# Optimization experiments

Measured on AMD Instinct MI355X. Metric: run time of the kernel, lower is better.

The kernel has to match this reference:

```python
import jax, jax.numpy as jnp
import numpy as np

Nc, Nt, B, L = 24, 1024, 32, 24
D = Nt // 4          # 256 encoder_output_dim
C16 = 16 * Nc        # 384 per-channel linears
H8 = 8 * Nc          # 192 LSTM hidden
WS = 0.02            # weight scale for numerical stability


def setup_inputs() -> dict:
    key = jax.random.key(0)
    ctr = [0]
    def nk():
        ctr[0] += 1
        return jax.random.fold_in(key, ctr[0])
    def rn(shape, s=WS):
        return jax.random.normal(nk(), shape, dtype=jnp.float32) * s
    def ru(shape):
        return jax.random.uniform(nk(), shape, dtype=jnp.float32)
    inp = {}
    inp["x"] = rn((B, 1, Nc, Nt), 1.0)
    inp["eps"] = rn((B, C16, L), 1.0)
    inp["sconv_w"] = rn((2 * Nc, 1, Nc, 1)); inp["sconv_b"] = rn((2 * Nc,))
    inp["tconv1_w"] = rn((4 * Nc, 2 * Nc, 1, 16)); inp["tconv1_b"] = rn((4 * Nc,))
    inp["tconv2_w"] = rn((8 * Nc, 4 * Nc, 1, 16)); inp["tconv2_b"] = rn((8 * Nc,))
    for i, c in ((1, 2 * Nc), (2, 4 * Nc), (3, 8 * Nc), (4, 4 * Nc), (5, 2 * Nc), (6, 2 * Nc)):
        inp[f"bn{i}_g"] = ru((c,)); inp[f"bn{i}_b"] = rn((c,))
        inp[f"bn{i}_m"] = jnp.zeros((c,), jnp.float32); inp[f"bn{i}_v"] = jnp.ones((c,), jnp.float32)
        inp[f"a{i}"] = ru((1,))
    for d in ("f", "b"):
        inp[f"w_ih_{d}"] = rn((4 * H8, H8)); inp[f"w_hh_{d}"] = rn((4 * H8, H8))
        inp[f"b_ih_{d}"] = rn((4 * H8,)); inp[f"b_hh_{d}"] = rn((4 * H8,))
    inp["mu_w"] = rn((C16, L, D)); inp["mu_b"] = rn((C16, L))
    inp["lv_w"] = rn((C16, L, D)); inp["lv_b"] = rn((C16, L))
    inp["dec_w"] = rn((C16, D, L)); inp["dec_b"] = rn((C16, D))
    inp["dconv1_w"] = rn((16 * Nc, 4 * Nc, 1, 16)); inp["dconv1_b"] = rn((4 * Nc,))
    inp["dconv2_w"] = rn((8 * Nc, 2 * Nc, 1, 16)); inp["dconv2_b"] = rn((2 * Nc,))
    inp["sdconv_w"] = rn((4 * Nc, 2 * Nc, Nc, 1)); inp["sdconv_b"] = rn((2 * Nc,))
    inp["fconv_w"] = rn((1, 2 * Nc, 1, 1)); inp["fconv_b"] = rn((1,))
    return inp


def _bn(x, g, b, m, v):
    scale = (g * jax.lax.rsqrt(v + 1e-5))[None, :, None, None]
    return (x - m[None, :, None, None]) * scale + b[None, :, None, None]


def _prelu(x, a):
    return jnp.where(x >= 0, x, a * x)


def _conv(x, w, b, stride, pad):
    y = jax.lax.conv_general_dilated(x, w, stride, pad,
                                     dimension_numbers=("NCHW", "OIHW", "NCHW"))
    return y + b[None, :, None, None]


def _convT(x, w, b, stride, pad, opad):
    # w in PyTorch ConvTranspose2d layout (Cin, Cout, kH, kW)
    w2 = jnp.flip(jnp.transpose(w, (1, 0, 2, 3)), (2, 3))
    kH, kW = w.shape[2], w.shape[3]
    padding = ((kH - 1 - pad[0], kH - 1 - pad[0] + opad[0]),
               (kW - 1 - pad[1], kW - 1 - pad[1] + opad[1]))
    y = jax.lax.conv_general_dilated(x, w2, (1, 1), padding, lhs_dilation=stride,
                                     dimension_numbers=("NCHW", "OIHW", "NCHW"))
    return y + b[None, :, None, None]


def _lstm_dir(xs, w_ih, w_hh, b_ih, b_hh, reverse):
    # xs: (T, B, In); PyTorch gate order i, f, g, o
    gx = jnp.einsum("tbi,gi->tbg", xs, w_ih) + (b_ih + b_hh)
    Bb, Hh = xs.shape[1], w_hh.shape[1]
    def step(carry, gt):
        h, c = carry
        gates = gt + h @ w_hh.T
        i, f, g, o = jnp.split(gates, 4, axis=-1)
        c = jax.nn.sigmoid(f) * c + jax.nn.sigmoid(i) * jnp.tanh(g)
        h = jax.nn.sigmoid(o) * jnp.tanh(c)
        return (h, c), h
    init = (jnp.zeros((Bb, Hh), xs.dtype), jnp.zeros((Bb, Hh), xs.dtype))
    _, hs = jax.lax.scan(step, init, gx, reverse=reverse)
    return hs  # (T, B, H), aligned with input time order


def _forward(p):
    # Encoder (dropout = identity, BN in eval mode)
    x1 = _prelu(_bn(_conv(p["x"], p["sconv_w"], p["sconv_b"], (Nc, 1), ((0, 0), (0, 0))),
                    p["bn1_g"], p["bn1_b"], p["bn1_m"], p["bn1_v"]), p["a1"])   # (B,2Nc,1,Nt)
    x2 = _prelu(_bn(_conv(x1, p["tconv1_w"], p["tconv1_b"], (1, 2), ((0, 0), (7, 7))),
                    p["bn2_g"], p["bn2_b"], p["bn2_m"], p["bn2_v"]), p["a2"])   # (B,4Nc,1,Nt/2)
    x3 = _prelu(_bn(_conv(x2, p["tconv2_w"], p["tconv2_b"], (1, 2), ((0, 0), (7, 7))),
                    p["bn3_g"], p["bn3_b"], p["bn3_m"], p["bn3_v"]), p["a3"])   # (B,8Nc,1,Nt/4)
    x3s = jnp.transpose(x3[:, :, 0, :], (2, 0, 1))                              # (T,B,8Nc)
    hf = _lstm_dir(x3s, p["w_ih_f"], p["w_hh_f"], p["b_ih_f"], p["b_hh_f"], False)
    hb = _lstm_dir(x3s, p["w_ih_b"], p["w_hh_b"], p["b_ih_b"], p["b_hh_b"], True)
    h = jnp.concatenate([hf, hb], axis=-1)                                      # (T,B,16Nc)
    h = h.reshape(D, x3.shape[0], H8, 2).mean(-1)                               # AvgPool1d(k=2) over feature dim
    tr = jnp.transpose(h, (1, 2, 0))                                            # (B,8Nc,T)
    e0 = jnp.concatenate([tr, x3[:, :, 0, :]], axis=1)                          # (B,16Nc,T=D)
    # 16*Nc per-channel Linears fused as batched GEMMs
    mu = jnp.einsum("bcd,cld->bcl", e0, p["mu_w"]) + p["mu_b"]                  # (B,384,L)
    logvar = jnp.einsum("bcd,cld->bcl", e0, p["lv_w"]) + p["lv_b"]
    z = mu + p["eps"] * jnp.exp(0.5 * logvar)
    x4 = (jnp.einsum("bcl,cdl->bcd", z, p["dec_w"]) + p["dec_b"])[:, :, None, :]  # (B,384,1,D)
    # Decoder (Nt%4==0 and Nt%2==0 -> output_padding 0)
    u1 = _prelu(_bn(_convT(x4, p["dconv1_w"], p["dconv1_b"], (1, 2), (0, 7), (0, 0)),
                    p["bn4_g"], p["bn4_b"], p["bn4_m"], p["bn4_v"]), p["a4"])   # (B,4Nc,1,Nt/2)
    e1 = jnp.concatenate([u1, x2], axis=1)                                      # (B,8Nc,1,Nt/2)
    u2 = _prelu(_bn(_convT(e1, p["dconv2_w"], p["dconv2_b"], (1, 2), (0, 7), (0, 0)),
                    p["bn5_g"], p["bn5_b"], p["bn5_m"], p["bn5_v"]), p["a5"])   # (B,2Nc,1,Nt)
    e2 = jnp.concatenate([u2, x1], axis=1)                                      # (B,4Nc,1,Nt)
    u3 = _prelu(_bn(_convT(e2, p["sdconv_w"], p["sdconv_b"], (Nc, 1), (0, 0), (0, 0)),
                    p["bn6_g"], p["bn6_b"], p["bn6_m"], p["bn6_v"]), p["a6"])   # (B,2Nc,Nc,Nt)
    out = _conv(u3, p["fconv_w"], p["fconv_b"], (1, 1), ((0, 0), (0, 0)))       # (B,1,Nc,Nt)
    return out, mu, logvar


def reference(x, eps, sconv_w, sconv_b, tconv1_w, tconv1_b, tconv2_w, tconv2_b,
              bn1_g, bn1_b, bn1_m, bn1_v, a1, bn2_g, bn2_b, bn2_m, bn2_v, a2,
              bn3_g, bn3_b, bn3_m, bn3_v, a3, bn4_g, bn4_b, bn4_m, bn4_v, a4,
              bn5_g, bn5_b, bn5_m, bn5_v, a5, bn6_g, bn6_b, bn6_m, bn6_v, a6,
              w_ih_f, w_hh_f, b_ih_f, b_hh_f, w_ih_b, w_hh_b, b_ih_b, b_hh_b,
              mu_w, mu_b, lv_w, lv_b, dec_w, dec_b,
              dconv1_w, dconv1_b, dconv2_w, dconv2_b, sdconv_w, sdconv_b,
              fconv_w, fconv_b):
    p = dict(locals())
    return _forward(p)
```

## Files before the change

### kernel.cpp

```cpp
#include <hip/hip_runtime.h>
#include <cstdint>

#define DI __device__ __forceinline__

typedef __attribute__((ext_vector_type(8))) short s8v;
typedef __attribute__((ext_vector_type(4))) float f4v;
typedef __attribute__((ext_vector_type(4))) uint32_t u4v;

DI float sigmoidf_(float x) {
    return __builtin_amdgcn_rcpf(1.f + __expf(-x));
}
DI float tanhf_(float x) {
    return fmaf(-2.f, __builtin_amdgcn_rcpf(1.f + __expf(2.f * x)), 1.f);
}
DI uint32_t f2bf(float f) {
    uint32_t u = __float_as_uint(f);
    return (u + 0x7fffu + ((u >> 16) & 1u)) >> 16;
}
DI float bflo(uint32_t u) { return __uint_as_float(u << 16); }
DI float bfhi(uint32_t u) { return __uint_as_float(u & 0xffff0000u); }

__global__ __launch_bounds__(256) void k_prep(
    const float* wihf, const float* wihb, const float* whhf, const float* whhb,
    const float* bihf, const float* bhhf, const float* bihb, const float* bhhb,
    const float* sdw,
    float* wihT, uint32_t* wfrag, float* bsum, float* wsdT)
{
    int i = blockIdx.x * 256 + threadIdx.x;
    if (i < 294912) {
        int d = i / 147456, r = i % 147456;
        int ii = r / 768, g = r % 768;
        const float* w = d ? wihb : wihf;
        wihT[i] = w[g * 192 + ii];
        return;
    }
    int j = i - 294912;
    if (j < 147456) {
        int d = j / 73728, r = j % 73728;
        int w = r / 6144, r2 = r % 6144;
        int tau = r2 / 1536, r3 = r2 % 1536;
        int kt = r3 / 256, r4 = r3 % 256;
        int lane = r4 / 4, jp = r4 % 4;
        int n = 16 * (w + 12 * tau) + (lane & 15);
        int k0 = kt * 32 + (lane >> 4) * 8 + jp * 2;
        const float* whh = d ? whhb : whhf;
        uint32_t lo = f2bf(whh[n * 192 + k0]);
        uint32_t hi = f2bf(whh[n * 192 + k0 + 1]);
        wfrag[j] = lo | (hi << 16);
        return;
    }
    int k = j - 147456;
    if (k < 1536) {
        int d = k / 768, g = k % 768;
        bsum[k] = d ? (bihb[g] + bhhb[g]) : (bihf[g] + bhhf[g]);
        return;
    }
    int l = k - 1536;
    if (l < 110592) {
        int h = l / 4608, rem = l % 4608;
        int co = rem / 96, ci = rem % 96;
        wsdT[l] = sdw[(ci * 48 + co) * 24 + h];
    }
}

__global__ __launch_bounds__(256) void k_sconv(
    const float* __restrict__ x, const float* __restrict__ w, const float* __restrict__ bias,
    const float* g, const float* bb, const float* m, const float* v, const float* a,
    float* __restrict__ x1)
{
    int t = blockIdx.x * 256 + threadIdx.x;
    int co = blockIdx.y;
    int b = blockIdx.z;
    const float* xb = x + (size_t)b * 24 * 1024 + t;
    float acc = bias[co];
#pragma unroll
    for (int h = 0; h < 24; ++h) acc = fmaf(xb[h * 1024], w[co * 24 + h], acc);
    float sc = g[co] * rsqrtf(v[co] + 1e-5f);
    float y = (acc - m[co]) * sc + bb[co];
    float al = a[0];
    y = y >= 0.f ? y : al * y;
    x1[((size_t)b * 48 + co) * 1024 + t] = y;
}

template<int CI, int CO, int WOUT, int BSTR>
__global__ __launch_bounds__(256) void k_tconv(
    const float* __restrict__ xin, const float* __restrict__ w, const float* __restrict__ bias,
    const float* g, const float* bb, const float* m, const float* v, const float* a,
    float* __restrict__ out)
{
    const int WIN = WOUT * 2;
    __shared__ float XL[CI][144];
    int tid = threadIdx.x;
    int w0 = blockIdx.x * 64;
    int b = blockIdx.z;
    for (int idx = tid; idx < CI * 144; idx += 256) {
        int ci = idx / 144, p = idx % 144;
        int gp = 2 * w0 - 7 + p;
        XL[ci][p] = (gp >= 0 && gp < WIN) ? xin[((size_t)b * CI + ci) * WIN + gp] : 0.f;
    }
    __syncthreads();
    int tw = tid & 63, cg = tid >> 6;
    int co0 = blockIdx.y * 16 + cg * 4;
    co0 = __builtin_amdgcn_readfirstlane(co0);
    const float* wb = w + (size_t)co0 * CI * 16;
    float acc[4] = {bias[co0], bias[co0 + 1], bias[co0 + 2], bias[co0 + 3]};
    for (int ci = 0; ci < CI; ++ci) {
#pragma unroll
        for (int k = 0; k < 16; ++k) {
            float xv = XL[ci][2 * tw + k];
            acc[0] = fmaf(xv, wb[(0 * CI + ci) * 16 + k], acc[0]);
            acc[1] = fmaf(xv, wb[(1 * CI + ci) * 16 + k], acc[1]);
            acc[2] = fmaf(xv, wb[(2 * CI + ci) * 16 + k], acc[2]);
            acc[3] = fmaf(xv, wb[(3 * CI + ci) * 16 + k], acc[3]);
        }
    }
    float al = a[0];
#pragma unroll
    for (int r = 0; r < 4; ++r) {
        int co = co0 + r;
        float sc = g[co] * rsqrtf(v[co] + 1e-5f);
        float y = (acc[r] - m[co]) * sc + bb[co];
        y = y >= 0.f ? y : al * y;
        out[((size_t)b * BSTR + co) * WOUT + w0 + tw] = y;
    }
}

__global__ __launch_bounds__(256) void k_x3s(const float* __restrict__ e0, float* __restrict__ x3s)
{
    __shared__ float tl[64 * 193];
    int t0 = blockIdx.x * 64, b = blockIdx.y;
    int tid = threadIdx.x;
    for (int idx = tid; idx < 192 * 64; idx += 256) {
        int i = idx >> 6, tt = idx & 63;
        tl[tt * 193 + i] = e0[((size_t)b * 384 + 192 + i) * 256 + t0 + tt];
    }
    __syncthreads();
    for (int idx = tid; idx < 64 * 192; idx += 256) {
        int tt = idx / 192, ii = idx % 192;
        x3s[((size_t)(t0 + tt) * 32 + b) * 192 + ii] = tl[tt * 193 + ii];
    }
}

__global__ __launch_bounds__(256) void k_gemm(
    const float* __restrict__ A, const float* __restrict__ Bm,
    const float* __restrict__ bias, float* __restrict__ C)
{
    __shared__ float AL[64 * 17];
    __shared__ float BL[16 * 68];
    int tid = threadIdx.x;
    int n0 = blockIdx.x * 64, m0 = blockIdx.y * 64;
    int tx = tid & 15, ty = tid >> 4;
    float4 cc[4] = {};
    for (int k0 = 0; k0 < 192; k0 += 16) {
        for (int idx = tid; idx < 1024; idx += 256) {
            int r = idx >> 4, c = idx & 15;
            AL[r * 17 + c] = A[(size_t)(m0 + r) * 192 + k0 + c];
        }
        for (int idx = tid; idx < 1024; idx += 256) {
            int kk = idx >> 6, jj = idx & 63;
            BL[kk * 68 + jj] = Bm[(size_t)(k0 + kk) * 768 + n0 + jj];
        }
        __syncthreads();
#pragma unroll
        for (int kk = 0; kk < 16; ++kk) {
            float4 b4 = *(const float4*)&BL[kk * 68 + tx * 4];
            float a0 = AL[(ty * 4 + 0) * 17 + kk];
            float a1 = AL[(ty * 4 + 1) * 17 + kk];
            float a2 = AL[(ty * 4 + 2) * 17 + kk];
            float a3 = AL[(ty * 4 + 3) * 17 + kk];
            cc[0].x = fmaf(a0, b4.x, cc[0].x); cc[0].y = fmaf(a0, b4.y, cc[0].y);
            cc[0].z = fmaf(a0, b4.z, cc[0].z); cc[0].w = fmaf(a0, b4.w, cc[0].w);
            cc[1].x = fmaf(a1, b4.x, cc[1].x); cc[1].y = fmaf(a1, b4.y, cc[1].y);
            cc[1].z = fmaf(a1, b4.z, cc[1].z); cc[1].w = fmaf(a1, b4.w, cc[1].w);
            cc[2].x = fmaf(a2, b4.x, cc[2].x); cc[2].y = fmaf(a2, b4.y, cc[2].y);
            cc[2].z = fmaf(a2, b4.z, cc[2].z); cc[2].w = fmaf(a2, b4.w, cc[2].w);
            cc[3].x = fmaf(a3, b4.x, cc[3].x); cc[3].y = fmaf(a3, b4.y, cc[3].y);
            cc[3].z = fmaf(a3, b4.z, cc[3].z); cc[3].w = fmaf(a3, b4.w, cc[3].w);
        }
        __syncthreads();
    }
    float4 bs = *(const float4*)&bias[n0 + tx * 4];
#pragma unroll
    for (int i = 0; i < 4; ++i) {
        float4 r = cc[i];
        r.x += bs.x; r.y += bs.y; r.z += bs.z; r.w += bs.w;
        *(float4*)&C[(size_t)(m0 + ty * 4 + i) * 768 + n0 + tx * 4] = r;
    }
}

__global__ __launch_bounds__(768, 3) void k_lstm_mfma(
    const float* __restrict__ gx, const short* __restrict__ wfrag,
    float* __restrict__ htmp)
{
    __shared__ __align__(16) short Hf[2][3072];

    int bid = blockIdx.x;
    int d = bid >> 1;
    int b0 = (bid & 1) * 16;
    int tid = threadIdx.x;
    int w = tid >> 6;
    int l = tid & 63;
    int lm = l & 15, lq = l >> 4;

    u4v Bw[4][6];
    {
        const short* wb = wfrag + ((size_t)(d * 12 + w) * 4) * 3072 + (size_t)l * 8;
#pragma unroll
        for (int tau = 0; tau < 4; ++tau)
#pragma unroll
            for (int kt = 0; kt < 6; ++kt)
                Bw[tau][kt] = *(const u4v*)(wb + (tau * 6 + kt) * 512);
    }
#pragma unroll
    for (int tau = 0; tau < 4; ++tau)
#pragma unroll
        for (int kt = 0; kt < 6; ++kt)
            asm volatile("" : "+v"(Bw[tau][kt]));

    for (int i2 = tid; i2 < 1536; i2 += 768) ((uint32_t*)Hf[0])[i2] = 0u;

    float c4[4] = {0.f, 0.f, 0.f, 0.f};

    const float* gxb = gx + (size_t)d * 6291456 + (size_t)(b0 + lq * 4) * 768 + w * 16 + lm;
    float pre[4][4];
    {
        int t0 = d ? 255 : 0;
        const float* gp = gxb + (size_t)t0 * 24576;
#pragma unroll
        for (int tau = 0; tau < 4; ++tau)
#pragma unroll
            for (int r = 0; r < 4; ++r)
                pre[tau][r] = gp[r * 768 + tau * 192];
    }

    int j = w * 16 + lm;
    int kt_j = j >> 5, kg_j = (j >> 3) & 3, off_j = j & 7;
    int hw_u32 = (kt_j * 512 + (kg_j * 16 + lq * 4) * 8 + (off_j & ~1)) >> 1;
    float* hbase = htmp + ((size_t)d * 256 * 32 + b0 + lm) * 96 + lq * 4;

    __syncthreads();

    for (int s = 0; s < 256; ++s) {
        int t = d ? 255 - s : s;
        int p = s & 1;
        f4v acc[4];
#pragma unroll
        for (int tau = 0; tau < 4; ++tau) {
            f4v a0 = {pre[tau][0], pre[tau][1], pre[tau][2], pre[tau][3]};
            acc[tau] = a0;
        }
        if (s < 255) {
            int tn = d ? 254 - s : s + 1;
            const float* gp = gxb + (size_t)tn * 24576;
#pragma unroll
            for (int tau = 0; tau < 4; ++tau)
#pragma unroll
                for (int r = 0; r < 4; ++r)
                    pre[tau][r] = gp[r * 768 + tau * 192];
        }
        bool dost = (w == 0) && (s > 0);
        int tprev = d ? t + 1 : t - 1;
        float* hst = hbase + (size_t)tprev * 3072;
#pragma unroll
        for (int kt = 0; kt < 6; ++kt) {
            s8v A = *(const s8v*)&Hf[p][kt * 512 + l * 8];
            if (dost) {
                const uint32_t* au = (const uint32_t*)&A;
                float4 pv;
                pv.x = 0.5f * (bflo(au[0]) + bfhi(au[0]));
                pv.y = 0.5f * (bflo(au[1]) + bfhi(au[1]));
                pv.z = 0.5f * (bflo(au[2]) + bfhi(au[2]));
                pv.w = 0.5f * (bflo(au[3]) + bfhi(au[3]));
                *(float4*)&hst[kt * 16] = pv;
            }
            acc[0] = __builtin_amdgcn_mfma_f32_16x16x32_bf16(
                A, __builtin_bit_cast(s8v, Bw[0][kt]), acc[0], 0, 0, 0);
            acc[1] = __builtin_amdgcn_mfma_f32_16x16x32_bf16(
                A, __builtin_bit_cast(s8v, Bw[1][kt]), acc[1], 0, 0, 0);
            acc[2] = __builtin_amdgcn_mfma_f32_16x16x32_bf16(
                A, __builtin_bit_cast(s8v, Bw[2][kt]), acc[2], 0, 0, 0);
            acc[3] = __builtin_amdgcn_mfma_f32_16x16x32_bf16(
                A, __builtin_bit_cast(s8v, Bw[3][kt]), acc[3], 0, 0, 0);
        }
        float hv[4];
#pragma unroll
        for (int r = 0; r < 4; ++r) {
            float ig = sigmoidf_(acc[0][r]);
            float fg = sigmoidf_(acc[1][r]);
            float gg = tanhf_(acc[2][r]);
            float og = sigmoidf_(acc[3][r]);
            c4[r] = fmaf(fg, c4[r], ig * gg);
            hv[r] = og * tanhf_(c4[r]);
        }
        float hp[4];
#pragma unroll
        for (int r = 0; r < 4; ++r) hp[r] = __shfl_xor(hv[r], 1);
        if ((lm & 1) == 0) {
            uint32_t* dst = (uint32_t*)Hf[p ^ 1];
#pragma unroll
            for (int r = 0; r < 4; ++r)
                dst[hw_u32 + r * 4] = f2bf(hv[r]) | (f2bf(hp[r]) << 16);
        }
        __syncthreads();
    }
    if (w == 0) {
        int tlast = d ? 0 : 255;
        float* hst = hbase + (size_t)tlast * 3072;
#pragma unroll
        for (int kt = 0; kt < 6; ++kt) {
            s8v A = *(const s8v*)&Hf[0][kt * 512 + l * 8];
            const uint32_t* au = (const uint32_t*)&A;
            float4 pv;
            pv.x = 0.5f * (bflo(au[0]) + bfhi(au[0]));
            pv.y = 0.5f * (bflo(au[1]) + bfhi(au[1]));
            pv.z = 0.5f * (bflo(au[2]) + bfhi(au[2]));
            pv.w = 0.5f * (bflo(au[3]) + bfhi(au[3]));
            *(float4*)&hst[kt * 16] = pv;
        }
    }
}

__global__ __launch_bounds__(256) void k_hT(const float* __restrict__ htmp, float* __restrict__ e0)
{
    __shared__ float tl[96 * 65];
    int t0 = blockIdx.x * 64;
    int b = blockIdx.y;
    int d = blockIdx.z;
    int tid = threadIdx.x;
    for (int idx = tid; idx < 6144; idx += 256) {
        int tt = idx / 96, jp = idx % 96;
        tl[jp * 65 + tt] = htmp[(((size_t)d * 256 + t0 + tt) * 32 + b) * 96 + jp];
    }
    __syncthreads();
    for (int idx = tid; idx < 6144; idx += 256) {
        int jp = idx >> 6, tt = idx & 63;
        e0[((size_t)b * 384 + d * 96 + jp) * 256 + t0 + tt] = tl[jp * 65 + tt];
    }
}

__global__ __launch_bounds__(256) void k_muz(
    const float* __restrict__ e0, const float* __restrict__ muw, const float* __restrict__ mub,
    const float* __restrict__ lvw, const float* __restrict__ lvb, const float* __restrict__ eps,
    float* __restrict__ mu_out, float* __restrict__ lv_out, float* __restrict__ z)
{
    int c = blockIdx.x;
    int tid = threadIdx.x;
    __shared__ float eL[32 * 257];
    __shared__ float gL[48 * 33];
    for (int idx = tid; idx < 8192; idx += 256) {
        int b = idx >> 8, dd = idx & 255;
        eL[b * 257 + dd] = e0[((size_t)b * 384 + c) * 256 + dd];
    }
    __syncthreads();
    for (int rep = 0; rep < 6; ++rep) {
        int task = rep * 256 + tid;
        int b = task & 31, r = task >> 5;
        const float* row = (r < 24) ? (muw + ((size_t)c * 24 + r) * 256)
                                    : (lvw + ((size_t)c * 24 + (r - 24)) * 256);
        float acc = 0.f;
#pragma unroll 4
        for (int dd = 0; dd < 256; ++dd) acc = fmaf(eL[b * 257 + dd], row[dd], acc);
        acc += (r < 24) ? mub[c * 24 + r] : lvb[c * 24 + (r - 24)];
        gL[r * 33 + b] = acc;
    }
    __syncthreads();
    for (int rep = 0; rep < 3; ++rep) {
        int task = rep * 256 + tid;
        int b = task / 24, l = task % 24;
        float muv = gL[l * 33 + b], lvv = gL[(24 + l) * 33 + b];
        size_t oi = ((size_t)b * 384 + c) * 24 + l;
        mu_out[oi] = muv;
        lv_out[oi] = lvv;
        z[oi] = fmaf(eps[oi], __expf(0.5f * lvv), muv);
    }
}

__global__ __launch_bounds__(256) void k_dec(
    const float* __restrict__ z, const float* __restrict__ dw, const float* __restrict__ db,
    float* __restrict__ x4)
{
    int c = blockIdx.x, tid = threadIdx.x;
    __shared__ float zL[32 * 25];
    __shared__ float WdL[256 * 25];
    for (int idx = tid; idx < 768; idx += 256) {
        int b = idx / 24, l = idx % 24;
        zL[b * 25 + l] = z[((size_t)b * 384 + c) * 24 + l];
    }
    for (int idx = tid; idx < 6144; idx += 256) {
        int dd = idx / 24, l = idx % 24;
        WdL[dd * 25 + l] = dw[((size_t)c * 256 + dd) * 24 + l];
    }
    __syncthreads();
    for (int rep = 0; rep < 32; ++rep) {
        int task = rep * 256 + tid;
        int b = task >> 8, dd = task & 255;
        float acc = db[c * 256 + dd];
#pragma unroll
        for (int l = 0; l < 24; ++l) acc = fmaf(zL[b * 25 + l], WdL[dd * 25 + l], acc);
        x4[((size_t)b * 384 + c) * 256 + dd] = acc;
    }
}

template<int CI, int CO, int WIN, int SPLIT, int COFULL>
__global__ __launch_bounds__(256) void k_convT(
    const float* __restrict__ in1, const float* __restrict__ in2, const float* __restrict__ w,
    const float* __restrict__ bias, const float* g, const float* bb, const float* m,
    const float* v, const float* a, float* __restrict__ out)
{
    const int WOUT = WIN * 2;
    constexpr int R = CO / 16;
    __shared__ float XL[8 * 41];
    __shared__ float WL[8 * CO * 18];
    int tid = threadIdx.x;
    int w0 = blockIdx.x * 64, b = blockIdx.z;
    int cb = blockIdx.y * CO;
    int u0 = w0 >> 1;
    int wq = tid & 15, cq = tid >> 4;
    float acc[4][R];
#pragma unroll
    for (int i = 0; i < 4; ++i)
#pragma unroll
        for (int r = 0; r < R; ++r) acc[i][r] = 0.f;

    for (int ci0 = 0; ci0 < CI; ci0 += 8) {
        __syncthreads();
        for (int idx = tid; idx < 320; idx += 256) {
            int ci = idx / 40, p = idx % 40;
            int dpos = u0 - 4 + p;
            int cig = ci0 + ci;
            float val = 0.f;
            if (dpos >= 0 && dpos < WIN)
                val = (cig < SPLIT) ? in1[((size_t)b * SPLIT + cig) * WIN + dpos]
                                    : in2[((size_t)b * (CI - SPLIT) + (cig - SPLIT)) * WIN + dpos];
            XL[ci * 41 + p] = val;
        }
        for (int idx = tid; idx < 8 * CO * 16; idx += 256) {
            int ci = idx / (CO * 16), rem = idx % (CO * 16);
            int co = rem / 16, k = rem & 15;
            WL[(ci * CO + co) * 18 + k] = w[((size_t)(ci0 + ci) * COFULL + cb + co) * 16 + k];
        }
        __syncthreads();
        for (int ci = 0; ci < 8; ++ci) {
            float xr[10];
#pragma unroll
            for (int p = 0; p < 10; ++p) xr[p] = XL[ci * 41 + 2 * wq + p];
#pragma unroll
            for (int j = 0; j < 8; ++j) {
                float xa = xr[7 - j];
                float xb = xr[8 - j];
                float xc = xr[9 - j];
#pragma unroll
                for (int r = 0; r < R; ++r) {
                    float2 wv = *(const float2*)&WL[(ci * CO + cq * R + r) * 18 + 2 * j];
                    acc[0][r] = fmaf(xa, wv.y, acc[0][r]);
                    acc[1][r] = fmaf(xb, wv.x, acc[1][r]);
                    acc[2][r] = fmaf(xb, wv.y, acc[2][r]);
                    acc[3][r] = fmaf(xc, wv.x, acc[3][r]);
                }
            }
        }
    }
    float al = a[0];
#pragma unroll
    for (int r = 0; r < R; ++r) {
        int co = cb + cq * R + r;
        float sc = g[co] * rsqrtf(v[co] + 1e-5f);
        float bi = bias[co], mm = m[co], be = bb[co];
        float4 yv;
        float* yf = (float*)&yv;
#pragma unroll
        for (int i = 0; i < 4; ++i) {
            float y = (acc[i][r] + bi - mm) * sc + be;
            yf[i] = y >= 0.f ? y : al * y;
        }
        *(float4*)&out[((size_t)b * COFULL + co) * WOUT + w0 + wq * 4] = yv;
    }
}

__global__ __launch_bounds__(256) void k_final(
    const float* __restrict__ u2, const float* __restrict__ x1, const float* __restrict__ wsdT,
    const float* __restrict__ sdb, const float* g, const float* bb, const float* m,
    const float* v, const float* a, const float* fcw, const float* fcb, float* __restrict__ out)
{
    __shared__ float e2L[64 * 100];
    __shared__ float WL[48 * 100];
    __shared__ float red[64 * 17];
    int tid = threadIdx.x;
    int t0 = blockIdx.x * 64, h = blockIdx.y, b = blockIdx.z;
    for (int idx = tid; idx < 6144; idx += 256) {
        int ci = idx >> 6, tt = idx & 63;
        float vv = (ci < 48) ? u2[((size_t)b * 48 + ci) * 1024 + t0 + tt]
                             : x1[((size_t)b * 48 + (ci - 48)) * 1024 + t0 + tt];
        e2L[tt * 100 + ci] = vv;
    }
    for (int idx = tid; idx < 4608; idx += 256) {
        WL[(idx / 96) * 100 + (idx % 96)] = wsdT[(size_t)h * 4608 + idx];
    }
    __syncthreads();
    int tx = tid & 15, ty = tid >> 4;
    float accv[4][3] = {};
    for (int c4 = 0; c4 < 24; ++c4) {
        float4 e4[4], w4[3];
#pragma unroll
        for (int i = 0; i < 4; ++i) e4[i] = *(const float4*)&e2L[(tx + 16 * i) * 100 + c4 * 4];
#pragma unroll
        for (int r = 0; r < 3; ++r) w4[r] = *(const float4*)&WL[(ty * 3 + r) * 100 + c4 * 4];
#pragma unroll
        for (int i = 0; i < 4; ++i)
#pragma unroll
            for (int r = 0; r < 3; ++r) {
                accv[i][r] = fmaf(e4[i].x, w4[r].x, accv[i][r]);
                accv[i][r] = fmaf(e4[i].y, w4[r].y, accv[i][r]);
                accv[i][r] = fmaf(e4[i].z, w4[r].z, accv[i][r]);
                accv[i][r] = fmaf(e4[i].w, w4[r].w, accv[i][r]);
            }
    }
    float al = a[0];
    float psum[4] = {};
#pragma unroll
    for (int r = 0; r < 3; ++r) {
        int co = ty * 3 + r;
        float sc = g[co] * rsqrtf(v[co] + 1e-5f);
        float fw = fcw[co], bi = sdb[co], mm = m[co], be = bb[co];
#pragma unroll
        for (int i = 0; i < 4; ++i) {
            float y = (accv[i][r] + bi - mm) * sc + be;
            y = y >= 0.f ? y : al * y;
            psum[i] = fmaf(fw, y, psum[i]);
        }
    }
#pragma unroll
    for (int i = 0; i < 4; ++i) red[(i * 16 + tx) * 17 + ty] = psum[i];
    __syncthreads();
    if (tid < 64) {
        float s = fcb[0];
#pragma unroll
        for (int y2 = 0; y2 < 16; ++y2) s += red[tid * 17 + y2];
        out[((size_t)b * 24 + h) * 1024 + t0 + tid] = s;
    }
}

extern "C" void kernel_launch(void* const* d_in, const int* in_sizes, int n_in,
                              void* d_out, int out_size, void* d_ws, size_t ws_size,
                              hipStream_t stream)
{
    (void)in_sizes; (void)n_in; (void)out_size; (void)ws_size;
    const float* x        = (const float*)d_in[0];
    const float* eps      = (const float*)d_in[1];
    const float* sconv_w  = (const float*)d_in[2];
    const float* sconv_b  = (const float*)d_in[3];
    const float* tconv1_w = (const float*)d_in[4];
    const float* tconv1_b = (const float*)d_in[5];
    const float* tconv2_w = (const float*)d_in[6];
    const float* tconv2_b = (const float*)d_in[7];
    const float *bn1g=(const float*)d_in[8],  *bn1b=(const float*)d_in[9],  *bn1m=(const float*)d_in[10], *bn1v=(const float*)d_in[11], *a1=(const float*)d_in[12];
    const float *bn2g=(const float*)d_in[13], *bn2b=(const float*)d_in[14], *bn2m=(const float*)d_in[15], *bn2v=(const float*)d_in[16], *a2=(const float*)d_in[17];
    const float *bn3g=(const float*)d_in[18], *bn3b=(const float*)d_in[19], *bn3m=(const float*)d_in[20], *bn3v=(const float*)d_in[21], *a3=(const float*)d_in[22];
    const float *bn4g=(const float*)d_in[23], *bn4b=(const float*)d_in[24], *bn4m=(const float*)d_in[25], *bn4v=(const float*)d_in[26], *a4=(const float*)d_in[27];
    const float *bn5g=(const float*)d_in[28], *bn5b=(const float*)d_in[29], *bn5m=(const float*)d_in[30], *bn5v=(const float*)d_in[31], *a5=(const float*)d_in[32];
    const float *bn6g=(const float*)d_in[33], *bn6b=(const float*)d_in[34], *bn6m=(const float*)d_in[35], *bn6v=(const float*)d_in[36], *a6=(const float*)d_in[37];
    const float *wihf=(const float*)d_in[38], *whhf=(const float*)d_in[39], *bihf=(const float*)d_in[40], *bhhf=(const float*)d_in[41];
    const float *wihb=(const float*)d_in[42], *whhb=(const float*)d_in[43], *bihb=(const float*)d_in[44], *bhhb=(const float*)d_in[45];
    const float *mu_w=(const float*)d_in[46], *mu_b=(const float*)d_in[47];
    const float *lv_w=(const float*)d_in[48], *lv_b=(const float*)d_in[49];
    const float *dec_w=(const float*)d_in[50], *dec_b=(const float*)d_in[51];
    const float *dconv1_w=(const float*)d_in[52], *dconv1_b=(const float*)d_in[53];
    const float *dconv2_w=(const float*)d_in[54], *dconv2_b=(const float*)d_in[55];
    const float *sdconv_w=(const float*)d_in[56], *sdconv_b=(const float*)d_in[57];
    const float *fconv_w=(const float*)d_in[58], *fconv_b=(const float*)d_in[59];

    float* ws = (float*)d_ws;
    float* x1   = ws + 0;
    float* x2   = ws + 1572864;
    float* e0   = ws + 3145728;
    float* x3s  = ws + 6291456;
    float* htmp = ws + 6291456;
    float* wihT = ws + 7864320;
    uint32_t* wfrag = (uint32_t*)(ws + 8159232);
    float* bsum = ws + 8306688;
    float* gx   = ws + 8308736;
    float* z    = ws + 8308736;
    float* x4   = ws + 8603648;
    float* u1   = ws + 11749376;
    float* u2   = ws + 13322240;
    float* wsdT = ws + 20891648;

    float* out0 = (float*)d_out;
    float* muo  = out0 + 786432;
    float* lvo  = muo + 294912;

    k_prep<<<2166, 256, 0, stream>>>(wihf, wihb, whhf, whhb, bihf, bhhf, bihb, bhhb,
                                     sdconv_w, wihT, wfrag, bsum, wsdT);
    k_sconv<<<dim3(4, 48, 32), 256, 0, stream>>>(x, sconv_w, sconv_b, bn1g, bn1b, bn1m, bn1v, a1, x1);
    k_tconv<48, 96, 512, 96><<<dim3(8, 6, 32), 256, 0, stream>>>(
        x1, tconv1_w, tconv1_b, bn2g, bn2b, bn2m, bn2v, a2, x2);
    k_tconv<96, 192, 256, 384><<<dim3(4, 12, 32), 256, 0, stream>>>(
        x2, tconv2_w, tconv2_b, bn3g, bn3b, bn3m, bn3v, a3, e0 + 49152);
    k_x3s<<<dim3(4, 32), 256, 0, stream>>>(e0, x3s);
    k_gemm<<<dim3(12, 128), 256, 0, stream>>>(x3s, wihT, bsum, gx);
    k_gemm<<<dim3(12, 128), 256, 0, stream>>>(x3s, wihT + 147456, bsum + 768, gx + 6291456);
    k_lstm_mfma<<<4, 768, 0, stream>>>(gx, (const short*)wfrag, htmp);
    k_hT<<<dim3(4, 32, 2), 256, 0, stream>>>(htmp, e0);
    k_muz<<<384, 256, 0, stream>>>(e0, mu_w, mu_b, lv_w, lv_b, eps, muo, lvo, z);
    k_dec<<<384, 256, 0, stream>>>(z, dec_w, dec_b, x4);
    k_convT<384, 48, 256, 384, 96><<<dim3(8, 2, 32), 256, 0, stream>>>(
        x4, x4, dconv1_w, dconv1_b, bn4g, bn4b, bn4m, bn4v, a4, u1);
    k_convT<192, 48, 512, 96, 48><<<dim3(16, 1, 32), 256, 0, stream>>>(
        u1, x2, dconv2_w, dconv2_b, bn5g, bn5b, bn5m, bn5v, a5, u2);
    k_final<<<dim3(16, 24, 32), 256, 0, stream>>>(
        u2, x1, wsdT, sdconv_b, bn6g, bn6b, bn6m, bn6v, a6, fconv_w, fconv_b, out0);
}
```

Before: 1.738 ms.

## Streamline LSTM recurrence barrier, spread h stores across waves, tile W_ih transpose

Replaces __syncthreads in the serial LSTM step loop with an explicit lgkmcnt wait plus s_barrier, so the barrier waits only on LDS traffic and not on outstanding global loads or stores. The h-state stores to global are now split across six waves (one kt slice each) instead of all being issued by wave 0. The gate-input prefetch uses incrementing pointers, and the register-pinning asm for the weights moves inside the loop. The W_ih transpose moves into a separate LDS-tiled kernel for coalesced access. This relies on global stores and prefetches not needing to complete before the barrier, which the data flow appears to allow.

```diff
diff --git a/kernel.cpp b/kernel.cpp
--- a/kernel.cpp
+++ b/kernel.cpp
@@ -19,24 +19,19 @@
 }
 DI float bflo(uint32_t u) { return __uint_as_float(u << 16); }
 DI float bfhi(uint32_t u) { return __uint_as_float(u & 0xffff0000u); }
+DI void lgkm_barrier() {
+    asm volatile("s_waitcnt lgkmcnt(0)\n\ts_barrier" ::: "memory");
+}
 
 __global__ __launch_bounds__(256) void k_prep(
-    const float* wihf, const float* wihb, const float* whhf, const float* whhb,
+    const float* whhf, const float* whhb,
     const float* bihf, const float* bhhf, const float* bihb, const float* bhhb,
     const float* sdw,
-    float* wihT, uint32_t* wfrag, float* bsum, float* wsdT)
+    uint32_t* wfrag, float* bsum, float* wsdT)
 {
     int i = blockIdx.x * 256 + threadIdx.x;
-    if (i < 294912) {
-        int d = i / 147456, r = i % 147456;
-        int ii = r / 768, g = r % 768;
-        const float* w = d ? wihb : wihf;
-        wihT[i] = w[g * 192 + ii];
-        return;
-    }
-    int j = i - 294912;
-    if (j < 147456) {
-        int d = j / 73728, r = j % 73728;
+    if (i < 147456) {
+        int d = i / 73728, r = i % 73728;
         int w = r / 6144, r2 = r % 6144;
         int tau = r2 / 1536, r3 = r2 % 1536;
         int kt = r3 / 256, r4 = r3 % 256;
@@ -46,10 +41,10 @@
         const float* whh = d ? whhb : whhf;
         uint32_t lo = f2bf(whh[n * 192 + k0]);
         uint32_t hi = f2bf(whh[n * 192 + k0 + 1]);
-        wfrag[j] = lo | (hi << 16);
+        wfrag[i] = lo | (hi << 16);
         return;
     }
-    int k = j - 147456;
+    int k = i - 147456;
     if (k < 1536) {
         int d = k / 768, g = k % 768;
         bsum[k] = d ? (bihb[g] + bhhb[g]) : (bihf[g] + bhhf[g]);
@@ -60,6 +55,24 @@
         int h = l / 4608, rem = l % 4608;
         int co = rem / 96, ci = rem % 96;
         wsdT[l] = sdw[(ci * 48 + co) * 24 + h];
+    }
+}
+
+__global__ __launch_bounds__(256) void k_prepT(
+    const float* wihf, const float* wihb, float* wihT)
+{
+    __shared__ float tl[64 * 65];
+    int ii0 = blockIdx.x * 64, g0 = blockIdx.y * 64, d = blockIdx.z;
+    const float* w = d ? wihb : wihf;
+    int tid = threadIdx.x;
+    for (int r = tid; r < 4096; r += 256) {
+        int gg = r >> 6, ii = r & 63;
+        tl[ii * 65 + gg] = w[(size_t)(g0 + gg) * 192 + ii0 + ii];
+    }
+    __syncthreads();
+    for (int r = tid; r < 4096; r += 256) {
+        int ii = r >> 6, gg = r & 63;
+        wihT[(size_t)d * 147456 + (size_t)(ii0 + ii) * 768 + g0 + gg] = tl[ii * 65 + gg];
     }
 }
 
@@ -211,12 +224,6 @@
             for (int kt = 0; kt < 6; ++kt)
                 Bw[tau][kt] = *(const u4v*)(wb + (tau * 6 + kt) * 512);
     }
-#pragma unroll
-    for (int tau = 0; tau < 4; ++tau)
-#pragma unroll
-        for (int kt = 0; kt < 6; ++kt)
-            asm volatile("" : "+v"(Bw[tau][kt]));
-
     for (int i2 = tid; i2 < 1536; i2 += 768) ((uint32_t*)Hf[0])[i2] = 0u;
 
     float c4[4] = {0.f, 0.f, 0.f, 0.f};
@@ -224,23 +231,35 @@
     const float* gxb = gx + (size_t)d * 6291456 + (size_t)(b0 + lq * 4) * 768 + w * 16 + lm;
     float pre[4][4];
     {
-        int t0 = d ? 255 : 0;
-        const float* gp = gxb + (size_t)t0 * 24576;
+        const float* gp = gxb + (size_t)(d ? 255 : 0) * 24576;
 #pragma unroll
         for (int tau = 0; tau < 4; ++tau)
 #pragma unroll
             for (int r = 0; r < 4; ++r)
                 pre[tau][r] = gp[r * 768 + tau * 192];
     }
+    ptrdiff_t dstep = d ? -24576 : 24576;
+    const float* pr0 = gxb + (size_t)(d ? 254 : 1) * 24576;
+    const float* pr1 = pr0 + 768;
+    const float* pr2 = pr0 + 1536;
+    const float* pr3 = pr0 + 2304;
 
     int j = w * 16 + lm;
     int kt_j = j >> 5, kg_j = (j >> 3) & 3, off_j = j & 7;
     int hw_u32 = (kt_j * 512 + (kg_j * 16 + lq * 4) * 8 + (off_j & ~1)) >> 1;
-    float* hbase = htmp + ((size_t)d * 256 * 32 + b0 + lm) * 96 + lq * 4;
+    float* hbase = htmp + ((size_t)d * 8192 + b0 + lm) * 96 + w * 16 + lq * 4;
 
     __syncthreads();
 
     for (int s = 0; s < 256; ++s) {
+        asm volatile("" : "+v"(Bw[0][0]), "+v"(Bw[0][1]), "+v"(Bw[0][2]),
+                          "+v"(Bw[0][3]), "+v"(Bw[0][4]), "+v"(Bw[0][5]));
+        asm volatile("" : "+v"(Bw[1][0]), "+v"(Bw[1][1]), "+v"(Bw[1][2]),
+                          "+v"(Bw[1][3]), "+v"(Bw[1][4]), "+v"(Bw[1][5]));
+        asm volatile("" : "+v"(Bw[2][0]), "+v"(Bw[2][1]), "+v"(Bw[2][2]),
+                          "+v"(Bw[2][3]), "+v"(Bw[2][4]), "+v"(Bw[2][5]));
+        asm volatile("" : "+v"(Bw[3][0]), "+v"(Bw[3][1]), "+v"(Bw[3][2]),
+                          "+v"(Bw[3][3]), "+v"(Bw[3][4]), "+v"(Bw[3][5]));
         int t = d ? 255 - s : s;
         int p = s & 1;
         f4v acc[4];
@@ -250,28 +269,29 @@
             acc[tau] = a0;
         }
         if (s < 255) {
-            int tn = d ? 254 - s : s + 1;
-            const float* gp = gxb + (size_t)tn * 24576;
-#pragma unroll
-            for (int tau = 0; tau < 4; ++tau)
-#pragma unroll
-                for (int r = 0; r < 4; ++r)
-                    pre[tau][r] = gp[r * 768 + tau * 192];
-        }
-        bool dost = (w == 0) && (s > 0);
+#pragma unroll
+            for (int tau = 0; tau < 4; ++tau) pre[tau][0] = pr0[tau * 192];
+#pragma unroll
+            for (int tau = 0; tau < 4; ++tau) pre[tau][1] = pr1[tau * 192];
+#pragma unroll
+            for (int tau = 0; tau < 4; ++tau) pre[tau][2] = pr2[tau * 192];
+#pragma unroll
+            for (int tau = 0; tau < 4; ++tau) pre[tau][3] = pr3[tau * 192];
+            pr0 += dstep; pr1 += dstep; pr2 += dstep; pr3 += dstep;
+        }
         int tprev = d ? t + 1 : t - 1;
         float* hst = hbase + (size_t)tprev * 3072;
 #pragma unroll
         for (int kt = 0; kt < 6; ++kt) {
             s8v A = *(const s8v*)&Hf[p][kt * 512 + l * 8];
-            if (dost) {
+            if (w == kt && s > 0) {
                 const uint32_t* au = (const uint32_t*)&A;
                 float4 pv;
                 pv.x = 0.5f * (bflo(au[0]) + bfhi(au[0]));
                 pv.y = 0.5f * (bflo(au[1]) + bfhi(au[1]));
                 pv.z = 0.5f * (bflo(au[2]) + bfhi(au[2]));
                 pv.w = 0.5f * (bflo(au[3]) + bfhi(au[3]));
-                *(float4*)&hst[kt * 16] = pv;
+                *(float4*)hst = pv;
             }
             acc[0] = __builtin_amdgcn_mfma_f32_16x16x32_bf16(
                 A, __builtin_bit_cast(s8v, Bw[0][kt]), acc[0], 0, 0, 0);
@@ -301,22 +321,19 @@
             for (int r = 0; r < 4; ++r)
                 dst[hw_u32 + r * 4] = f2bf(hv[r]) | (f2bf(hp[r]) << 16);
         }
-        __syncthreads();
-    }
-    if (w == 0) {
+        lgkm_barrier();
+    }
+    if (w < 6) {
         int tlast = d ? 0 : 255;
         float* hst = hbase + (size_t)tlast * 3072;
-#pragma unroll
-        for (int kt = 0; kt < 6; ++kt) {
-            s8v A = *(const s8v*)&Hf[0][kt * 512 + l * 8];
-            const uint32_t* au = (const uint32_t*)&A;
-            float4 pv;
-            pv.x = 0.5f * (bflo(au[0]) + bfhi(au[0]));
-            pv.y = 0.5f * (bflo(au[1]) + bfhi(au[1]));
-            pv.z = 0.5f * (bflo(au[2]) + bfhi(au[2]));
-            pv.w = 0.5f * (bflo(au[3]) + bfhi(au[3]));
-            *(float4*)&hst[kt * 16] = pv;
-        }
+        s8v A = *(const s8v*)&Hf[0][w * 512 + l * 8];
+        const uint32_t* au = (const uint32_t*)&A;
+        float4 pv;
+        pv.x = 0.5f * (bflo(au[0]) + bfhi(au[0]));
+        pv.y = 0.5f * (bflo(au[1]) + bfhi(au[1]));
+        pv.z = 0.5f * (bflo(au[2]) + bfhi(au[2]));
+        pv.w = 0.5f * (bflo(au[3]) + bfhi(au[3]));
+        *(float4*)hst = pv;
     }
 }
 
@@ -589,8 +606,9 @@
     float* muo  = out0 + 786432;
     float* lvo  = muo + 294912;
 
-    k_prep<<<2166, 256, 0, stream>>>(wihf, wihb, whhf, whhb, bihf, bhhf, bihb, bhhb,
-                                     sdconv_w, wihT, wfrag, bsum, wsdT);
+    k_prep<<<1014, 256, 0, stream>>>(whhf, whhb, bihf, bhhf, bihb, bhhb,
+                                     sdconv_w, wfrag, bsum, wsdT);
+    k_prepT<<<dim3(3, 12, 2), 256, 0, stream>>>(wihf, wihb, wihT);
     k_sconv<<<dim3(4, 48, 32), 256, 0, stream>>>(x, sconv_w, sconv_b, bn1g, bn1b, bn1m, bn1v, a1, x1);
     k_tconv<48, 96, 512, 96><<<dim3(8, 6, 32), 256, 0, stream>>>(
         x1, tconv1_w, tconv1_b, bn2g, bn2b, bn2m, bn2v, a2, x2);
```

Result: faster. 1.655 ms (-4.8%).
